# Kernel optimization log

Measured on AMD Instinct MI355X. Metric: run time of the kernel, lower is better.

## Reference

```python
import jax, jax.numpy as jnp
import numpy as np

NEG_SLOPE = 0.2
EPS = 1e-16


def _add_self_loops(edge_index, num_nodes):
    loop = jnp.arange(num_nodes, dtype=edge_index.dtype)
    return jnp.concatenate([edge_index, jnp.stack([loop, loop])], axis=1)


def gat_conv(x, edge_index, W, a_src, a_dst, b, concat):
    """PyG-style GATConv: gather -> attention logits -> segment softmax -> scatter-add."""
    N = x.shape[0]
    H, C = a_src.shape
    xl = (x @ W).reshape(N, H, C)                       # [N,H,C]
    alpha_src = (xl * a_src[None]).sum(-1)              # [N,H]
    alpha_dst = (xl * a_dst[None]).sum(-1)              # [N,H]
    src, dst = edge_index[0], edge_index[1]
    alpha = jax.nn.leaky_relu(alpha_src[src] + alpha_dst[dst], NEG_SLOPE)  # [E,H]
    amax = jax.ops.segment_max(alpha, dst, num_segments=N)
    amax = jnp.where(jnp.isfinite(amax), amax, 0.0)
    ea = jnp.exp(alpha - amax[dst])
    denom = jax.ops.segment_sum(ea, dst, num_segments=N)
    attn = ea / (denom[dst] + EPS)                      # [E,H]
    msg = xl[src] * attn[:, :, None]                    # [E,H,C]
    out = jax.ops.segment_sum(msg, dst, num_segments=N)  # [N,H,C]
    out = out.reshape(N, H * C) if concat else out.mean(axis=1)
    return out + b


def setup_inputs() -> dict:
    key = jax.random.key(0)
    ks = jax.random.split(key, 9)
    N, F, E, H, C, NC = 100000, 128, 1600000, 8, 8, 40
    s = lambda fan: 1.0 / np.sqrt(fan)
    return {
        "x": jax.random.normal(ks[0], (N, F), dtype=jnp.float32),
        "edge_index": jax.random.randint(ks[1], (2, E), 0, N, dtype=jnp.int64),
        "W1": jax.random.normal(ks[2], (F, H * C), dtype=jnp.float32) * s(F),
        "a_src1": jax.random.normal(ks[3], (H, C), dtype=jnp.float32) * s(C),
        "a_dst1": jax.random.normal(ks[4], (H, C), dtype=jnp.float32) * s(C),
        "b1": jnp.zeros((H * C,), dtype=jnp.float32),
        "W2": jax.random.normal(ks[5], (H * C, NC), dtype=jnp.float32) * s(H * C),
        "a_src2": jax.random.normal(ks[6], (1, NC), dtype=jnp.float32) * s(NC),
        "a_dst2": jax.random.normal(ks[7], (1, NC), dtype=jnp.float32) * s(NC),
        "b2": jnp.zeros((NC,), dtype=jnp.float32),
    }


def reference(x, edge_index, W1, a_src1, a_dst1, b1, W2, a_src2, a_dst2, b2):
    N = x.shape[0]
    ei = _add_self_loops(edge_index, N)
    h = gat_conv(x, ei, W1, a_src1, a_dst1, b1, concat=True)   # [N,64]
    h = jax.nn.elu(h)
    out = gat_conv(h, ei, W2, a_src2, a_dst2, b2, concat=True)  # [N,nclass]
    return out
```

## Files before the change

kernel.cpp:

```cpp
#include <hip/hip_runtime.h>
#include <math.h>

#define NEG_SLOPE 0.2f
#define GAT_EPS 1e-16f
#define LOG2E 1.44269504088896340736f

#define CH   2048
#define NBK  512

__device__ __forceinline__ unsigned pack_bf16(float a, float b) {
    unsigned ua = __float_as_uint(a);
    unsigned ub = __float_as_uint(b);
    ua = (ua + 0x8000u) >> 16;
    ub = (ub + 0x8000u) & 0xffff0000u;
    return ua | ub;
}
__device__ __forceinline__ float bf_lo(unsigned pk) {
    return __uint_as_float(pk << 16);
}
__device__ __forceinline__ float bf_hi(unsigned pk) {
    return __uint_as_float(pk & 0xffff0000u);
}


__global__ __launch_bounds__(256) void k_off_a(
    const int* __restrict__ cnt, int* __restrict__ off,
    int* __restrict__ tot, int NCHv)
{
    __shared__ int sm[256];
    int b = blockIdx.x;
    int t = threadIdx.x;
    int carry = 0;
    for (int c0 = 0; c0 < NCHv; c0 += 256) {
        int c = c0 + t;
        int v = (c < NCHv) ? cnt[c * NBK + b] : 0;
        sm[t] = v;
        __syncthreads();
        for (int o = 1; o < 256; o <<= 1) {
            int add = (t >= o) ? sm[t - o] : 0;
            __syncthreads();
            sm[t] += add;
            __syncthreads();
        }
        if (c < NCHv) off[c * NBK + b] = carry + sm[t] - v;
        carry += sm[255];
        __syncthreads();
    }
    if (t == 0) tot[b] = carry;
}

__global__ __launch_bounds__(256) void k_place(
    const int* __restrict__ ei, int E, int N, int shift,
    const int* __restrict__ off, const int* __restrict__ tot,
    unsigned* __restrict__ bslab)
{
    __shared__ int cur[NBK];
    __shared__ int ps[256];
    int c = blockIdx.x;
    int t = threadIdx.x;
    int carry = 0;
    for (int b0 = 0; b0 < NBK; b0 += 256) {
        int v = tot[b0 + t];
        ps[t] = v;
        __syncthreads();
        for (int o = 1; o < 256; o <<= 1) {
            int u = (t >= o) ? ps[t - o] : 0;
            __syncthreads();
            ps[t] += u;
            __syncthreads();
        }
        cur[b0 + t] = carry + ps[t] - v + off[(size_t)c * NBK + b0 + t];
        carry += ps[255];
        __syncthreads();
    }
    __syncthreads();

    int Etot = E + N;
    int base = c * CH;
    int lim = min(base + CH, Etot);
    int mask = (1 << shift) - 1;
    for (int e = base + t; e < lim; e += 256) {
        int s, d;
        if (e < E) { s = ei[e]; d = ei[E + e]; }
        else       { s = e - E; d = s; }
        int b = d >> shift;
        int pos = atomicAdd(&cur[b], 1);
        bslab[pos] = (unsigned)s | ((unsigned)(d & mask) << 17);
    }
}

__global__ __launch_bounds__(256) void k_csr2(
    const int* __restrict__ tot, const unsigned* __restrict__ bslab,
    int shift, int* __restrict__ row_ptr, int* __restrict__ csr_src,
    int N, int Etot)
{
    __shared__ int sdeg[1024];
    __shared__ int scur[1024];
    __shared__ int ps[256];
    __shared__ int bb[NBK + 1];
    int b = blockIdx.x;
    int tid = threadIdx.x;

    int carry = 0;
    for (int b0 = 0; b0 < NBK; b0 += 256) {
        int v = tot[b0 + tid];
        ps[tid] = v;
        __syncthreads();
        for (int o = 1; o < 256; o <<= 1) {
            int u = (tid >= o) ? ps[tid - o] : 0;
            __syncthreads();
            ps[tid] += u;
            __syncthreads();
        }
        bb[b0 + tid] = carry + ps[tid] - v;
        carry += ps[255];
        __syncthreads();
    }
    if (tid == 0) bb[NBK] = carry;
    __syncthreads();

    int beg = bb[b], end = bb[b + 1];
    int nodes = 1 << shift;
    int node0 = b << shift;
    for (int i = tid; i < nodes; i += 256) sdeg[i] = 0;
    __syncthreads();
    for (int i = beg + tid; i < end; i += 256)
        atomicAdd(&sdeg[bslab[i] >> 17], 1);
    __syncthreads();
    int per = (nodes + 255) / 256;
    int mybase = tid * per;
    int sum = 0;
    for (int j = 0; j < per; j++) sum += sdeg[mybase + j];
    ps[tid] = sum;
    __syncthreads();
    int v0 = ps[tid];
    for (int o = 1; o < 256; o <<= 1) {
        int v = (tid >= o) ? ps[tid - o] : 0;
        __syncthreads();
        ps[tid] += v;
        __syncthreads();
    }
    int run = ps[tid] - v0;
    for (int j = 0; j < per; j++) {
        int i = mybase + j;
        int dgi = sdeg[i];
        scur[i] = beg + run;
        int node = node0 + i;
        if (node < N) row_ptr[node] = beg + run;
        run += dgi;
    }
    if (b == 0 && tid == 0) row_ptr[N] = Etot;
    __syncthreads();
    for (int i = beg + tid; i < end; i += 256) {
        unsigned w = bslab[i];
        int pos = atomicAdd(&scur[w >> 17], 1);
        csr_src[pos] = (int)(w & 0x1FFFFu);
    }
}

__device__ __forceinline__ void emit_node1(
    const float* acc, int n, int q, int c0,
    const float* asrc, const float* adst,
    unsigned* __restrict__ xl1b, float* __restrict__ as1,
    float* __restrict__ ad1)
{
    uint4 pk0, pk1;
    pk0.x = pack_bf16(acc[0], acc[1]);  pk0.y = pack_bf16(acc[2], acc[3]);
    pk0.z = pack_bf16(acc[4], acc[5]);  pk0.w = pack_bf16(acc[6], acc[7]);
    pk1.x = pack_bf16(acc[8], acc[9]);  pk1.y = pack_bf16(acc[10], acc[11]);
    pk1.z = pack_bf16(acc[12], acc[13]); pk1.w = pack_bf16(acc[14], acc[15]);
    uint4* xo = (uint4*)(xl1b + (size_t)n * 32 + q * 8);
    xo[0] = pk0;
    xo[1] = pk1;
#pragma unroll
    for (int hh = 0; hh < 2; hh++) {
        float s = 0.0f, t = 0.0f;
#pragma unroll
        for (int c = 0; c < 8; c++) {
            s = fmaf(acc[hh * 8 + c], asrc[c0 + hh * 8 + c], s);
            t = fmaf(acc[hh * 8 + c], adst[c0 + hh * 8 + c], t);
        }
        as1[(size_t)n * 8 + 2 * q + hh] = s * LOG2E;
        ad1[(size_t)n * 8 + 2 * q + hh] = t * LOG2E;
    }
}

__global__ __launch_bounds__(256) void k_gemm1(
    const float* __restrict__ x, const float* __restrict__ W1,
    const float* __restrict__ a_src1, const float* __restrict__ a_dst1,
    unsigned* __restrict__ xl1b, float* __restrict__ as1,
    float* __restrict__ ad1, int N, int F,
    const int* __restrict__ ei, int E, int shift, int NCHv,
    int* __restrict__ cnt)
{
    __shared__ float Ws[128 * 64];
    __shared__ float asrc[64];
    __shared__ float adst[64];
    __shared__ int hist[NBK];

    if (blockIdx.x < NCHv) {
        for (int i = threadIdx.x; i < NBK; i += 256) hist[i] = 0;
        __syncthreads();
        int Etot = E + N;
        int base = blockIdx.x * CH;
        int lim = min(base + CH, Etot);
        for (int e = base + threadIdx.x; e < lim; e += 256) {
            int d = (e < E) ? ei[E + e] : (e - E);
            atomicAdd(&hist[d >> shift], 1);
        }
        __syncthreads();
        for (int i = threadIdx.x; i < NBK; i += 256)
            cnt[(size_t)blockIdx.x * NBK + i] = hist[i];
    }
    if (blockIdx.x * 256 >= N) return;

    for (int i = threadIdx.x; i < F * 64; i += 256) Ws[i] = W1[i];
    if (threadIdx.x < 64) {
        asrc[threadIdx.x] = a_src1[threadIdx.x];
        adst[threadIdx.x] = a_dst1[threadIdx.x];
    }
    __syncthreads();

    int q = threadIdx.x & 3;
    int n0 = blockIdx.x * 256 + (threadIdx.x >> 2) * 4;
    if (n0 >= N) return;
    int c0 = q * 16;
    int n1 = min(n0 + 1, N - 1);
    int n2 = min(n0 + 2, N - 1);
    int n3 = min(n0 + 3, N - 1);

    float acc0[16], acc1[16], acc2[16], acc3[16];
#pragma unroll
    for (int c = 0; c < 16; c++) { acc0[c]=0.f; acc1[c]=0.f; acc2[c]=0.f; acc3[c]=0.f; }

    const float4* xr0 = (const float4*)(x + (size_t)n0 * F);
    const float4* xr1 = (const float4*)(x + (size_t)n1 * F);
    const float4* xr2 = (const float4*)(x + (size_t)n2 * F);
    const float4* xr3 = (const float4*)(x + (size_t)n3 * F);

#define GEMM1_ROW(comp, ridx)                                        \
    { const float* w = &Ws[(k4 * 4 + ridx) * 64 + c0];               \
      _Pragma("unroll")                                              \
      for (int c = 0; c < 16; c++) {                                 \
          float wc = w[c];                                           \
          acc0[c] = fmaf(xv0.comp, wc, acc0[c]);                     \
          acc1[c] = fmaf(xv1.comp, wc, acc1[c]);                     \
          acc2[c] = fmaf(xv2.comp, wc, acc2[c]);                     \
          acc3[c] = fmaf(xv3.comp, wc, acc3[c]); } }

    for (int k4 = 0; k4 < F / 4; k4++) {
        float4 xv0 = xr0[k4];
        float4 xv1 = xr1[k4];
        float4 xv2 = xr2[k4];
        float4 xv3 = xr3[k4];
        GEMM1_ROW(x, 0)
        GEMM1_ROW(y, 1)
        GEMM1_ROW(z, 2)
        GEMM1_ROW(w, 3)
    }
#undef GEMM1_ROW

    emit_node1(acc0, n0, q, c0, asrc, adst, xl1b, as1, ad1);
    if (n0 + 1 < N) emit_node1(acc1, n0 + 1, q, c0, asrc, adst, xl1b, as1, ad1);
    if (n0 + 2 < N) emit_node1(acc2, n0 + 2, q, c0, asrc, adst, xl1b, as1, ad1);
    if (n0 + 3 < N) emit_node1(acc3, n0 + 3, q, c0, asrc, adst, xl1b, as1, ad1);
}

__global__ __launch_bounds__(256) void k_agg1(
    const int* __restrict__ row_ptr, const int* __restrict__ csr_src,
    const float* __restrict__ as1, const float* __restrict__ ad1,
    const unsigned* __restrict__ xl1b, const float* __restrict__ b1,
    float* __restrict__ h1, int N)
{
    int d = blockIdx.x * 8 + ((threadIdx.x >> 6) << 1) + ((threadIdx.x >> 5) & 1);
    if (d >= N) return;
    int lane = threadIdx.x & 31;
    int g = lane >> 3;
    int l = lane & 7;

    int beg = row_ptr[d], end = row_ptr[d + 1];
    float adh = ad1[(size_t)d * 8 + l];

    float ax[8];
#pragma unroll
    for (int j = 0; j < 8; j++) ax[j] = 0.f;
    float den = 0.f;

    int i = beg + g;
    for (; i + 4 < end; i += 8) {
        int s0 = csr_src[i];
        int s1 = csr_src[i + 4];
        size_t q0 = (size_t)s0 * 8 + l;
        size_t q1 = (size_t)s1 * 8 + l;
        float al0 = as1[q0] + adh;
        float al1 = as1[q1] + adh;
        uint4 k0 = *(const uint4*)(xl1b + (q0 << 2));
        uint4 k1 = *(const uint4*)(xl1b + (q1 << 2));
        al0 = fmaxf(al0, NEG_SLOPE * al0);
        al1 = fmaxf(al1, NEG_SLOPE * al1);
        float e0 = __builtin_amdgcn_exp2f(al0);
        float e1 = __builtin_amdgcn_exp2f(al1);
        ax[0] = fmaf(e0, bf_lo(k0.x), ax[0]);
        ax[1] = fmaf(e0, bf_hi(k0.x), ax[1]);
        ax[2] = fmaf(e0, bf_lo(k0.y), ax[2]);
        ax[3] = fmaf(e0, bf_hi(k0.y), ax[3]);
        ax[4] = fmaf(e0, bf_lo(k0.z), ax[4]);
        ax[5] = fmaf(e0, bf_hi(k0.z), ax[5]);
        ax[6] = fmaf(e0, bf_lo(k0.w), ax[6]);
        ax[7] = fmaf(e0, bf_hi(k0.w), ax[7]);
        ax[0] = fmaf(e1, bf_lo(k1.x), ax[0]);
        ax[1] = fmaf(e1, bf_hi(k1.x), ax[1]);
        ax[2] = fmaf(e1, bf_lo(k1.y), ax[2]);
        ax[3] = fmaf(e1, bf_hi(k1.y), ax[3]);
        ax[4] = fmaf(e1, bf_lo(k1.z), ax[4]);
        ax[5] = fmaf(e1, bf_hi(k1.z), ax[5]);
        ax[6] = fmaf(e1, bf_lo(k1.w), ax[6]);
        ax[7] = fmaf(e1, bf_hi(k1.w), ax[7]);
        den += e0 + e1;
    }
    if (i < end) {
        int s0 = csr_src[i];
        size_t q0 = (size_t)s0 * 8 + l;
        float al0 = as1[q0] + adh;
        uint4 k0 = *(const uint4*)(xl1b + (q0 << 2));
        al0 = fmaxf(al0, NEG_SLOPE * al0);
        float e0 = __builtin_amdgcn_exp2f(al0);
        ax[0] = fmaf(e0, bf_lo(k0.x), ax[0]);
        ax[1] = fmaf(e0, bf_hi(k0.x), ax[1]);
        ax[2] = fmaf(e0, bf_lo(k0.y), ax[2]);
        ax[3] = fmaf(e0, bf_hi(k0.y), ax[3]);
        ax[4] = fmaf(e0, bf_lo(k0.z), ax[4]);
        ax[5] = fmaf(e0, bf_hi(k0.z), ax[5]);
        ax[6] = fmaf(e0, bf_lo(k0.w), ax[6]);
        ax[7] = fmaf(e0, bf_hi(k0.w), ax[7]);
        den += e0;
    }

#pragma unroll
    for (int m = 8; m < 32; m <<= 1) {
#pragma unroll
        for (int j = 0; j < 8; j++) ax[j] += __shfl_xor(ax[j], m);
        den += __shfl_xor(den, m);
    }

    if (g == 0) {
        float inv = __builtin_amdgcn_rcpf(den + GAT_EPS);
        const float4* bb = (const float4*)(b1 + l * 8);
        float4 b0 = bb[0], b1v = bb[1];
        float4 o0, o1;
        float v;
        v = fmaf(ax[0], inv, b0.x);  o0.x = v > 0.f ? v : __expf(v) - 1.f;
        v = fmaf(ax[1], inv, b0.y);  o0.y = v > 0.f ? v : __expf(v) - 1.f;
        v = fmaf(ax[2], inv, b0.z);  o0.z = v > 0.f ? v : __expf(v) - 1.f;
        v = fmaf(ax[3], inv, b0.w);  o0.w = v > 0.f ? v : __expf(v) - 1.f;
        v = fmaf(ax[4], inv, b1v.x); o1.x = v > 0.f ? v : __expf(v) - 1.f;
        v = fmaf(ax[5], inv, b1v.y); o1.y = v > 0.f ? v : __expf(v) - 1.f;
        v = fmaf(ax[6], inv, b1v.z); o1.z = v > 0.f ? v : __expf(v) - 1.f;
        v = fmaf(ax[7], inv, b1v.w); o1.w = v > 0.f ? v : __expf(v) - 1.f;
        float4* op = (float4*)(h1 + (size_t)d * 64 + l * 8);
        op[0] = o0;
        op[1] = o1;
    }
}

__global__ __launch_bounds__(256) void k_node2(
    const float* __restrict__ h1, const float* __restrict__ W2,
    const float* __restrict__ a_src2, const float* __restrict__ a_dst2,
    unsigned* __restrict__ xl2b, float* __restrict__ ad2, int N)
{
    __shared__ float Ws[64 * 40];
    __shared__ float a2s[40];
    __shared__ float a2d[40];
    for (int i = threadIdx.x; i < 64 * 40; i += 256) Ws[i] = W2[i];
    if (threadIdx.x < 40) {
        a2s[threadIdx.x] = a_src2[threadIdx.x];
        a2d[threadIdx.x] = a_dst2[threadIdx.x];
    }
    __syncthreads();

    int q = threadIdx.x & 1;
    int n0 = blockIdx.x * 256 + (threadIdx.x >> 1) * 2;
    if (n0 >= N) return;
    int c0 = q * 20;
    int n1 = min(n0 + 1, N - 1);

    float o0[20], o1[20];
#pragma unroll
    for (int j = 0; j < 20; j++) { o0[j] = 0.f; o1[j] = 0.f; }

    const float4* hr0 = (const float4*)(h1 + (size_t)n0 * 64);
    const float4* hr1 = (const float4*)(h1 + (size_t)n1 * 64);

#define NODE2_ROW(comp, ridx)                                        \
    { const float* w = &Ws[(k4 * 4 + ridx) * 40 + c0];               \
      _Pragma("unroll")                                              \
      for (int j = 0; j < 20; j++) {                                 \
          float wj = w[j];                                           \
          o0[j] = fmaf(ha.comp, wj, o0[j]);                          \
          o1[j] = fmaf(hb.comp, wj, o1[j]); } }

    for (int k4 = 0; k4 < 16; k4++) {
        float4 ha = hr0[k4];
        float4 hb = hr1[k4];
        NODE2_ROW(x, 0)
        NODE2_ROW(y, 1)
        NODE2_ROW(z, 2)
        NODE2_ROW(w, 3)
    }
#undef NODE2_ROW

    float s0 = 0.f, t0 = 0.f, s1 = 0.f, t1 = 0.f;
#pragma unroll
    for (int j = 0; j < 20; j++) {
        s0 = fmaf(o0[j], a2s[c0 + j], s0);
        t0 = fmaf(o0[j], a2d[c0 + j], t0);
        s1 = fmaf(o1[j], a2s[c0 + j], s1);
        t1 = fmaf(o1[j], a2d[c0 + j], t1);
    }
    s0 += __shfl_xor(s0, 1);
    t0 += __shfl_xor(t0, 1);
    s1 += __shfl_xor(s1, 1);
    t1 += __shfl_xor(t1, 1);
    if (q == 0) {
        xl2b[(size_t)n0 * 24 + 20] = __float_as_uint(s0 * LOG2E);
        ad2[n0] = t0 * LOG2E;
        if (n0 + 1 < N) {
            xl2b[(size_t)(n0 + 1) * 24 + 20] = __float_as_uint(s1 * LOG2E);
            ad2[n0 + 1] = t1 * LOG2E;
        }
    }

    unsigned* xo0 = xl2b + (size_t)n0 * 24 + q * 10;
#pragma unroll
    for (int p = 0; p < 10; p++) xo0[p] = pack_bf16(o0[2 * p], o0[2 * p + 1]);
    if (n0 + 1 < N) {
        unsigned* xo1 = xl2b + (size_t)(n0 + 1) * 24 + q * 10;
#pragma unroll
        for (int p = 0; p < 10; p++) xo1[p] = pack_bf16(o1[2 * p], o1[2 * p + 1]);
    }
}

__global__ __launch_bounds__(256) void k_agg2(
    const int* __restrict__ row_ptr, const int* __restrict__ csr_src,
    const float* __restrict__ ad2,
    const unsigned* __restrict__ xl2b, const float* __restrict__ b2,
    float* __restrict__ out, int N)
{
    int d = blockIdx.x * 8 + ((threadIdx.x >> 6) << 1) + ((threadIdx.x >> 5) & 1);
    if (d >= N) return;
    int lane = threadIdx.x & 31;
    int g = lane >> 3;
    int l = lane & 7;
    if (l >= 5) return;

    int beg = row_ptr[d], end = row_ptr[d + 1];
    float add = ad2[d];

    float ax[8];
#pragma unroll
    for (int j = 0; j < 8; j++) ax[j] = 0.f;
    float den = 0.f;

    int i = beg + g;
    for (; i + 4 < end; i += 8) {
        int s0 = csr_src[i];
        int s1 = csr_src[i + 4];
        const unsigned* r0 = xl2b + (size_t)s0 * 24;
        const unsigned* r1 = xl2b + (size_t)s1 * 24;
        float al0 = __uint_as_float(r0[20]) + add;
        float al1 = __uint_as_float(r1[20]) + add;
        uint4 k0 = *(const uint4*)(r0 + l * 4);
        uint4 k1 = *(const uint4*)(r1 + l * 4);
        al0 = fmaxf(al0, NEG_SLOPE * al0);
        al1 = fmaxf(al1, NEG_SLOPE * al1);
        float e0 = __builtin_amdgcn_exp2f(al0);
        float e1 = __builtin_amdgcn_exp2f(al1);
        ax[0] = fmaf(e0, bf_lo(k0.x), ax[0]);
        ax[1] = fmaf(e0, bf_hi(k0.x), ax[1]);
        ax[2] = fmaf(e0, bf_lo(k0.y), ax[2]);
        ax[3] = fmaf(e0, bf_hi(k0.y), ax[3]);
        ax[4] = fmaf(e0, bf_lo(k0.z), ax[4]);
        ax[5] = fmaf(e0, bf_hi(k0.z), ax[5]);
        ax[6] = fmaf(e0, bf_lo(k0.w), ax[6]);
        ax[7] = fmaf(e0, bf_hi(k0.w), ax[7]);
        ax[0] = fmaf(e1, bf_lo(k1.x), ax[0]);
        ax[1] = fmaf(e1, bf_hi(k1.x), ax[1]);
        ax[2] = fmaf(e1, bf_lo(k1.y), ax[2]);
        ax[3] = fmaf(e1, bf_hi(k1.y), ax[3]);
        ax[4] = fmaf(e1, bf_lo(k1.z), ax[4]);
        ax[5] = fmaf(e1, bf_hi(k1.z), ax[5]);
        ax[6] = fmaf(e1, bf_lo(k1.w), ax[6]);
        ax[7] = fmaf(e1, bf_hi(k1.w), ax[7]);
        den += e0 + e1;
    }
    if (i < end) {
        int s0 = csr_src[i];
        const unsigned* r0 = xl2b + (size_t)s0 * 24;
        float al0 = __uint_as_float(r0[20]) + add;
        uint4 k0 = *(const uint4*)(r0 + l * 4);
        al0 = fmaxf(al0, NEG_SLOPE * al0);
        float e0 = __builtin_amdgcn_exp2f(al0);
        ax[0] = fmaf(e0, bf_lo(k0.x), ax[0]);
        ax[1] = fmaf(e0, bf_hi(k0.x), ax[1]);
        ax[2] = fmaf(e0, bf_lo(k0.y), ax[2]);
        ax[3] = fmaf(e0, bf_hi(k0.y), ax[3]);
        ax[4] = fmaf(e0, bf_lo(k0.z), ax[4]);
        ax[5] = fmaf(e0, bf_hi(k0.z), ax[5]);
        ax[6] = fmaf(e0, bf_lo(k0.w), ax[6]);
        ax[7] = fmaf(e0, bf_hi(k0.w), ax[7]);
        den += e0;
    }

#pragma unroll
    for (int m = 8; m < 32; m <<= 1) {
#pragma unroll
        for (int j = 0; j < 8; j++) ax[j] += __shfl_xor(ax[j], m);
        den += __shfl_xor(den, m);
    }

    if (g == 0) {
        float inv = __builtin_amdgcn_rcpf(den + GAT_EPS);
        float* op = out + (size_t)d * 40 + l * 8;
        const float* bb = b2 + l * 8;
#pragma unroll
        for (int j = 0; j < 8; j++) op[j] = fmaf(ax[j], inv, bb[j]);
    }
}

extern "C" void kernel_launch(void* const* d_in, const int* in_sizes, int n_in,
                              void* d_out, int out_size, void* d_ws, size_t ws_size,
                              hipStream_t stream) {
    const float* x      = (const float*)d_in[0];
    const int*   ei     = (const int*)d_in[1];
    const float* W1     = (const float*)d_in[2];
    const float* a_src1 = (const float*)d_in[3];
    const float* a_dst1 = (const float*)d_in[4];
    const float* b1     = (const float*)d_in[5];
    const float* W2     = (const float*)d_in[6];
    const float* a_src2 = (const float*)d_in[7];
    const float* a_dst2 = (const float*)d_in[8];
    const float* b2     = (const float*)d_in[9];

    int F = in_sizes[2] / 64;
    int N = in_sizes[0] / F;
    int E = in_sizes[1] / 2;
    int Etot = E + N;
    int NCHv = (Etot + CH - 1) / CH;
    int shift = 8;
    while (((N - 1) >> shift) >= NBK) shift++;

    unsigned* xl1b    = (unsigned*)d_ws;
    float*    h1      = (float*)(xl1b + (size_t)N * 32);
    float*    as1     = h1 + (size_t)N * 64;
    float*    ad1     = as1 + (size_t)N * 8;
    int*      row_ptr = (int*)(ad1 + (size_t)N * 8);
    int*      csr_src = row_ptr + (N + 1);
    unsigned* bslab   = (unsigned*)(csr_src + Etot);
    int*      cnt     = (int*)h1;
    int*      off     = cnt + (size_t)NCHv * NBK;
    int*      tot     = off + (size_t)NCHv * NBK;
    unsigned* xl2b    = xl1b;
    float*    ad2     = ad1;

    int gridG1 = (N + 255) / 256;
    if (gridG1 < NCHv) gridG1 = NCHv;
    k_gemm1<<<gridG1, 256, 0, stream>>>(x, W1, a_src1, a_dst1,
                                        xl1b, as1, ad1, N, F,
                                        ei, E, shift, NCHv, cnt);

    k_off_a<<<NBK, 256, 0, stream>>>(cnt, off, tot, NCHv);
    k_place<<<NCHv, 256, 0, stream>>>(ei, E, N, shift, off, tot, bslab);
    k_csr2 <<<NBK, 256, 0, stream>>>(tot, bslab, shift,
                                     row_ptr, csr_src, N, Etot);

    k_agg1 <<<(N + 7) / 8, 256, 0, stream>>>(row_ptr, csr_src, as1, ad1,
                                             xl1b, b1, h1, N);

    k_node2<<<(N + 255) / 256, 256, 0, stream>>>(h1, W2, a_src2, a_dst2,
                                                 xl2b, ad2, N);
    k_agg2 <<<(N + 7) / 8, 256, 0, stream>>>(row_ptr, csr_src, ad2,
                                             xl2b, b2, (float*)d_out, N);
}
```

Before: 293.0 us.

## Replace bucketed two-level CSR build with global-atomic degree count and scatter

Swaps the two-pass bucket sort (per-chunk histograms, offset scan, slab placement, per-bucket local sort) for a direct CSR build. Per-node degrees are counted with global atomics inside the first GEMM kernel, followed by a three-kernel scan and a scatter that uses one global atomicAdd per edge on a per-node cursor. This drops the intermediate slab and the extra pass over it, at the cost of many contended global atomics and a nondeterministic neighbor order within rows. It also adds a memset and more small kernel launches.

```diff
diff --git a/kernel.cpp b/kernel.cpp
--- a/kernel.cpp
+++ b/kernel.cpp
@@ -4,9 +4,6 @@
 #define NEG_SLOPE 0.2f
 #define GAT_EPS 1e-16f
 #define LOG2E 1.44269504088896340736f
-
-#define CH   2048
-#define NBK  512
 
 __device__ __forceinline__ unsigned pack_bf16(float a, float b) {
     unsigned ua = __float_as_uint(a);
@@ -23,138 +20,69 @@
 }
 
 
-__global__ __launch_bounds__(256) void k_off_a(
-    const int* __restrict__ cnt, int* __restrict__ off,
-    int* __restrict__ tot, int NCHv)
+__global__ __launch_bounds__(256) void k_scan1(
+    const int* __restrict__ deg, int* __restrict__ row_ptr,
+    int* __restrict__ bsum, int N)
 {
     __shared__ int sm[256];
-    int b = blockIdx.x;
     int t = threadIdx.x;
-    int carry = 0;
-    for (int c0 = 0; c0 < NCHv; c0 += 256) {
-        int c = c0 + t;
-        int v = (c < NCHv) ? cnt[c * NBK + b] : 0;
-        sm[t] = v;
+    int d = blockIdx.x * 256 + t;
+    int v = (d < N) ? deg[d] + 1 : 0;
+    sm[t] = v;
+    __syncthreads();
+    for (int o = 1; o < 256; o <<= 1) {
+        int u = (t >= o) ? sm[t - o] : 0;
         __syncthreads();
-        for (int o = 1; o < 256; o <<= 1) {
-            int add = (t >= o) ? sm[t - o] : 0;
-            __syncthreads();
-            sm[t] += add;
-            __syncthreads();
-        }
-        if (c < NCHv) off[c * NBK + b] = carry + sm[t] - v;
-        carry += sm[255];
+        sm[t] += u;
         __syncthreads();
     }
-    if (t == 0) tot[b] = carry;
-}
-
-__global__ __launch_bounds__(256) void k_place(
-    const int* __restrict__ ei, int E, int N, int shift,
-    const int* __restrict__ off, const int* __restrict__ tot,
-    unsigned* __restrict__ bslab)
-{
-    __shared__ int cur[NBK];
-    __shared__ int ps[256];
-    int c = blockIdx.x;
+    if (d < N) row_ptr[d] = sm[t] - v;
+    if (t == 255) bsum[blockIdx.x] = sm[255];
+}
+
+__global__ __launch_bounds__(512) void k_scan2(
+    const int* __restrict__ bsum, int* __restrict__ bases, int NB,
+    int* __restrict__ row_ptr, int N, int Etot)
+{
+    __shared__ int sm[512];
     int t = threadIdx.x;
-    int carry = 0;
-    for (int b0 = 0; b0 < NBK; b0 += 256) {
-        int v = tot[b0 + t];
-        ps[t] = v;
+    int v = (t < NB) ? bsum[t] : 0;
+    sm[t] = v;
+    __syncthreads();
+    for (int o = 1; o < 512; o <<= 1) {
+        int u = (t >= o) ? sm[t - o] : 0;
         __syncthreads();
-        for (int o = 1; o < 256; o <<= 1) {
-            int u = (t >= o) ? ps[t - o] : 0;
-            __syncthreads();
-            ps[t] += u;
-            __syncthreads();
-        }
-        cur[b0 + t] = carry + ps[t] - v + off[(size_t)c * NBK + b0 + t];
-        carry += ps[255];
+        sm[t] += u;
         __syncthreads();
     }
-    __syncthreads();
-
+    if (t < NB) bases[t] = sm[t] - v;
+    if (t == 0) row_ptr[N] = Etot;
+}
+
+__global__ __launch_bounds__(256) void k_fix(
+    const int* __restrict__ bases, int* __restrict__ row_ptr,
+    int* __restrict__ cur, int N)
+{
+    int d = blockIdx.x * 256 + threadIdx.x;
+    if (d < N) {
+        int r = bases[blockIdx.x] + row_ptr[d];
+        row_ptr[d] = r;
+        cur[d] = r;
+    }
+}
+
+__global__ __launch_bounds__(256) void k_scatter(
+    const int* __restrict__ ei, int E, int N,
+    int* __restrict__ cur, int* __restrict__ csr_src)
+{
     int Etot = E + N;
-    int base = c * CH;
-    int lim = min(base + CH, Etot);
-    int mask = (1 << shift) - 1;
-    for (int e = base + t; e < lim; e += 256) {
+    int stride = gridDim.x * 256;
+    for (int e = blockIdx.x * 256 + threadIdx.x; e < Etot; e += stride) {
         int s, d;
         if (e < E) { s = ei[e]; d = ei[E + e]; }
         else       { s = e - E; d = s; }
-        int b = d >> shift;
-        int pos = atomicAdd(&cur[b], 1);
-        bslab[pos] = (unsigned)s | ((unsigned)(d & mask) << 17);
-    }
-}
-
-__global__ __launch_bounds__(256) void k_csr2(
-    const int* __restrict__ tot, const unsigned* __restrict__ bslab,
-    int shift, int* __restrict__ row_ptr, int* __restrict__ csr_src,
-    int N, int Etot)
-{
-    __shared__ int sdeg[1024];
-    __shared__ int scur[1024];
-    __shared__ int ps[256];
-    __shared__ int bb[NBK + 1];
-    int b = blockIdx.x;
-    int tid = threadIdx.x;
-
-    int carry = 0;
-    for (int b0 = 0; b0 < NBK; b0 += 256) {
-        int v = tot[b0 + tid];
-        ps[tid] = v;
-        __syncthreads();
-        for (int o = 1; o < 256; o <<= 1) {
-            int u = (tid >= o) ? ps[tid - o] : 0;
-            __syncthreads();
-            ps[tid] += u;
-            __syncthreads();
-        }
-        bb[b0 + tid] = carry + ps[tid] - v;
-        carry += ps[255];
-        __syncthreads();
-    }
-    if (tid == 0) bb[NBK] = carry;
-    __syncthreads();
-
-    int beg = bb[b], end = bb[b + 1];
-    int nodes = 1 << shift;
-    int node0 = b << shift;
-    for (int i = tid; i < nodes; i += 256) sdeg[i] = 0;
-    __syncthreads();
-    for (int i = beg + tid; i < end; i += 256)
-        atomicAdd(&sdeg[bslab[i] >> 17], 1);
-    __syncthreads();
-    int per = (nodes + 255) / 256;
-    int mybase = tid * per;
-    int sum = 0;
-    for (int j = 0; j < per; j++) sum += sdeg[mybase + j];
-    ps[tid] = sum;
-    __syncthreads();
-    int v0 = ps[tid];
-    for (int o = 1; o < 256; o <<= 1) {
-        int v = (tid >= o) ? ps[tid - o] : 0;
-        __syncthreads();
-        ps[tid] += v;
-        __syncthreads();
-    }
-    int run = ps[tid] - v0;
-    for (int j = 0; j < per; j++) {
-        int i = mybase + j;
-        int dgi = sdeg[i];
-        scur[i] = beg + run;
-        int node = node0 + i;
-        if (node < N) row_ptr[node] = beg + run;
-        run += dgi;
-    }
-    if (b == 0 && tid == 0) row_ptr[N] = Etot;
-    __syncthreads();
-    for (int i = beg + tid; i < end; i += 256) {
-        unsigned w = bslab[i];
-        int pos = atomicAdd(&scur[w >> 17], 1);
-        csr_src[pos] = (int)(w & 0x1FFFFu);
+        int pos = atomicAdd(&cur[d], 1);
+        csr_src[pos] = s;
     }
 }
 
@@ -190,29 +118,19 @@
     const float* __restrict__ a_src1, const float* __restrict__ a_dst1,
     unsigned* __restrict__ xl1b, float* __restrict__ as1,
     float* __restrict__ ad1, int N, int F,
-    const int* __restrict__ ei, int E, int shift, int NCHv,
-    int* __restrict__ cnt)
+    const int* __restrict__ ei, int E, int* __restrict__ deg)
 {
     __shared__ float Ws[128 * 64];
     __shared__ float asrc[64];
     __shared__ float adst[64];
-    __shared__ int hist[NBK];
-
-    if (blockIdx.x < NCHv) {
-        for (int i = threadIdx.x; i < NBK; i += 256) hist[i] = 0;
-        __syncthreads();
-        int Etot = E + N;
-        int base = blockIdx.x * CH;
-        int lim = min(base + CH, Etot);
-        for (int e = base + threadIdx.x; e < lim; e += 256) {
-            int d = (e < E) ? ei[E + e] : (e - E);
-            atomicAdd(&hist[d >> shift], 1);
-        }
-        __syncthreads();
-        for (int i = threadIdx.x; i < NBK; i += 256)
-            cnt[(size_t)blockIdx.x * NBK + i] = hist[i];
-    }
-    if (blockIdx.x * 256 >= N) return;
+
+    {
+        int per = (E + (int)gridDim.x - 1) / (int)gridDim.x;
+        int base = blockIdx.x * per;
+        int lim = min(base + per, E);
+        for (int e = base + threadIdx.x; e < lim; e += 256)
+            atomicAdd(&deg[ei[E + e]], 1);
+    }
 
     for (int i = threadIdx.x; i < F * 64; i += 256) Ws[i] = W1[i];
     if (threadIdx.x < 64) {
@@ -545,9 +463,7 @@
     int N = in_sizes[0] / F;
     int E = in_sizes[1] / 2;
     int Etot = E + N;
-    int NCHv = (Etot + CH - 1) / CH;
-    int shift = 8;
-    while (((N - 1) >> shift) >= NBK) shift++;
+    int NB = (N + 255) / 256;
 
     unsigned* xl1b    = (unsigned*)d_ws;
     float*    h1      = (float*)(xl1b + (size_t)N * 32);
@@ -555,29 +471,31 @@
     float*    ad1     = as1 + (size_t)N * 8;
     int*      row_ptr = (int*)(ad1 + (size_t)N * 8);
     int*      csr_src = row_ptr + (N + 1);
-    unsigned* bslab   = (unsigned*)(csr_src + Etot);
-    int*      cnt     = (int*)h1;
-    int*      off     = cnt + (size_t)NCHv * NBK;
-    int*      tot     = off + (size_t)NCHv * NBK;
+    int*      deg     = csr_src + Etot;
+    int*      cur     = deg + N;
+    int*      bsum    = cur + N;
+    int*      bases   = bsum + NB;
     unsigned* xl2b    = xl1b;
     float*    ad2     = ad1;
 
-    int gridG1 = (N + 255) / 256;
-    if (gridG1 < NCHv) gridG1 = NCHv;
-    k_gemm1<<<gridG1, 256, 0, stream>>>(x, W1, a_src1, a_dst1,
-                                        xl1b, as1, ad1, N, F,
-                                        ei, E, shift, NCHv, cnt);
-
-    k_off_a<<<NBK, 256, 0, stream>>>(cnt, off, tot, NCHv);
-    k_place<<<NCHv, 256, 0, stream>>>(ei, E, N, shift, off, tot, bslab);
-    k_csr2 <<<NBK, 256, 0, stream>>>(tot, bslab, shift,
-                                     row_ptr, csr_src, N, Etot);
+    hipMemsetAsync(deg, 0, (size_t)N * sizeof(int), stream);
+
+    k_gemm1<<<NB, 256, 0, stream>>>(x, W1, a_src1, a_dst1,
+                                    xl1b, as1, ad1, N, F, ei, E, deg);
+
+    k_scan1<<<NB, 256, 0, stream>>>(deg, row_ptr, bsum, N);
+    k_scan2<<<1, 512, 0, stream>>>(bsum, bases, NB, row_ptr, N, Etot);
+    k_fix  <<<NB, 256, 0, stream>>>(bases, row_ptr, cur, N);
+    {
+        int gs = (Etot + 255) / 256;
+        if (gs > 2048) gs = 2048;
+        k_scatter<<<gs, 256, 0, stream>>>(ei, E, N, cur, csr_src);
+    }
 
     k_agg1 <<<(N + 7) / 8, 256, 0, stream>>>(row_ptr, csr_src, as1, ad1,
                                              xl1b, b1, h1, N);
 
-    k_node2<<<(N + 255) / 256, 256, 0, stream>>>(h1, W2, a_src2, a_dst2,
-                                                 xl2b, ad2, N);
+    k_node2<<<NB, 256, 0, stream>>>(h1, W2, a_src2, a_dst2, xl2b, ad2, N);
     k_agg2 <<<(N + 7) / 8, 256, 0, stream>>>(row_ptr, csr_src, ad2,
                                              xl2b, b2, (float*)d_out, N);
 }
```

Result: slower. 450.7 us (+53.8%).

## Fuse layer-2 linear projection into layer-1 aggregation epilogue

Applied to the files above, without the earlier changes.

Merges the k_node2 GEMM into the end of k_agg1. Each 32-lane destination group applies bias and ELU, multiplies by W2 held in shared memory, and reduces partial sums with shuffles to produce bf16 xl2 rows and the attention logits. This removes the fp32 h1 round-trip through global memory and one kernel launch. The cost is a W2 load into LDS in every small 8-node block, extra shuffle reductions, and xl2b/ad2 moving to separate workspace regions so they no longer alias xl1b and ad1 while those are still being read.

```diff
diff --git a/kernel.cpp b/kernel.cpp
--- a/kernel.cpp
+++ b/kernel.cpp
@@ -270,8 +270,22 @@
     const int* __restrict__ row_ptr, const int* __restrict__ csr_src,
     const float* __restrict__ as1, const float* __restrict__ ad1,
     const unsigned* __restrict__ xl1b, const float* __restrict__ b1,
-    float* __restrict__ h1, int N)
-{
+    const float* __restrict__ W2, const float* __restrict__ a_src2,
+    const float* __restrict__ a_dst2,
+    unsigned* __restrict__ xl2b, float* __restrict__ ad2, int N)
+{
+    __shared__ float W2s[64 * 40];
+    __shared__ float b1s[64];
+    __shared__ float a2ss[40];
+    __shared__ float a2ds[40];
+    for (int i = threadIdx.x; i < 64 * 40; i += 256) W2s[i] = W2[i];
+    if (threadIdx.x < 64) b1s[threadIdx.x] = b1[threadIdx.x];
+    if (threadIdx.x < 40) {
+        a2ss[threadIdx.x] = a_src2[threadIdx.x];
+        a2ds[threadIdx.x] = a_dst2[threadIdx.x];
+    }
+    __syncthreads();
+
     int d = blockIdx.x * 8 + ((threadIdx.x >> 6) << 1) + ((threadIdx.x >> 5) & 1);
     if (d >= N) return;
     int lane = threadIdx.x & 31;
@@ -343,100 +357,49 @@
         den += __shfl_xor(den, m);
     }
 
-    if (g == 0) {
-        float inv = __builtin_amdgcn_rcpf(den + GAT_EPS);
-        const float4* bb = (const float4*)(b1 + l * 8);
-        float4 b0 = bb[0], b1v = bb[1];
-        float4 o0, o1;
-        float v;
-        v = fmaf(ax[0], inv, b0.x);  o0.x = v > 0.f ? v : __expf(v) - 1.f;
-        v = fmaf(ax[1], inv, b0.y);  o0.y = v > 0.f ? v : __expf(v) - 1.f;
-        v = fmaf(ax[2], inv, b0.z);  o0.z = v > 0.f ? v : __expf(v) - 1.f;
-        v = fmaf(ax[3], inv, b0.w);  o0.w = v > 0.f ? v : __expf(v) - 1.f;
-        v = fmaf(ax[4], inv, b1v.x); o1.x = v > 0.f ? v : __expf(v) - 1.f;
-        v = fmaf(ax[5], inv, b1v.y); o1.y = v > 0.f ? v : __expf(v) - 1.f;
-        v = fmaf(ax[6], inv, b1v.z); o1.z = v > 0.f ? v : __expf(v) - 1.f;
-        v = fmaf(ax[7], inv, b1v.w); o1.w = v > 0.f ? v : __expf(v) - 1.f;
-        float4* op = (float4*)(h1 + (size_t)d * 64 + l * 8);
-        op[0] = o0;
-        op[1] = o1;
-    }
-}
-
-__global__ __launch_bounds__(256) void k_node2(
-    const float* __restrict__ h1, const float* __restrict__ W2,
-    const float* __restrict__ a_src2, const float* __restrict__ a_dst2,
-    unsigned* __restrict__ xl2b, float* __restrict__ ad2, int N)
-{
-    __shared__ float Ws[64 * 40];
-    __shared__ float a2s[40];
-    __shared__ float a2d[40];
-    for (int i = threadIdx.x; i < 64 * 40; i += 256) Ws[i] = W2[i];
-    if (threadIdx.x < 40) {
-        a2s[threadIdx.x] = a_src2[threadIdx.x];
-        a2d[threadIdx.x] = a_dst2[threadIdx.x];
-    }
-    __syncthreads();
-
-    int q = threadIdx.x & 1;
-    int n0 = blockIdx.x * 256 + (threadIdx.x >> 1) * 2;
-    if (n0 >= N) return;
-    int c0 = q * 20;
-    int n1 = min(n0 + 1, N - 1);
-
-    float o0[20], o1[20];
-#pragma unroll
-    for (int j = 0; j < 20; j++) { o0[j] = 0.f; o1[j] = 0.f; }
-
-    const float4* hr0 = (const float4*)(h1 + (size_t)n0 * 64);
-    const float4* hr1 = (const float4*)(h1 + (size_t)n1 * 64);
-
-#define NODE2_ROW(comp, ridx)                                        \
-    { const float* w = &Ws[(k4 * 4 + ridx) * 40 + c0];               \
-      _Pragma("unroll")                                              \
-      for (int j = 0; j < 20; j++) {                                 \
-          float wj = w[j];                                           \
-          o0[j] = fmaf(ha.comp, wj, o0[j]);                          \
-          o1[j] = fmaf(hb.comp, wj, o1[j]); } }
-
-    for (int k4 = 0; k4 < 16; k4++) {
-        float4 ha = hr0[k4];
-        float4 hb = hr1[k4];
-        NODE2_ROW(x, 0)
-        NODE2_ROW(y, 1)
-        NODE2_ROW(z, 2)
-        NODE2_ROW(w, 3)
-    }
-#undef NODE2_ROW
-
-    float s0 = 0.f, t0 = 0.f, s1 = 0.f, t1 = 0.f;
-#pragma unroll
-    for (int j = 0; j < 20; j++) {
-        s0 = fmaf(o0[j], a2s[c0 + j], s0);
-        t0 = fmaf(o0[j], a2d[c0 + j], t0);
-        s1 = fmaf(o1[j], a2s[c0 + j], s1);
-        t1 = fmaf(o1[j], a2d[c0 + j], t1);
-    }
-    s0 += __shfl_xor(s0, 1);
-    t0 += __shfl_xor(t0, 1);
-    s1 += __shfl_xor(s1, 1);
-    t1 += __shfl_xor(t1, 1);
-    if (q == 0) {
-        xl2b[(size_t)n0 * 24 + 20] = __float_as_uint(s0 * LOG2E);
-        ad2[n0] = t0 * LOG2E;
-        if (n0 + 1 < N) {
-            xl2b[(size_t)(n0 + 1) * 24 + 20] = __float_as_uint(s1 * LOG2E);
-            ad2[n0 + 1] = t1 * LOG2E;
+    float inv = __builtin_amdgcn_rcpf(den + GAT_EPS);
+    float h[8];
+#pragma unroll
+    for (int j = 0; j < 8; j++) {
+        float v = fmaf(ax[j], inv, b1s[l * 8 + j]);
+        h[j] = v > 0.f ? v : __expf(v) - 1.f;
+    }
+
+    float pt[10];
+#pragma unroll
+    for (int jj = 0; jj < 10; jj++) pt[jj] = 0.f;
+#pragma unroll
+    for (int c = 0; c < 8; c++) {
+        float hc = h[c];
+        const float* wr = &W2s[(l * 8 + c) * 40 + g * 10];
+#pragma unroll
+        for (int jj = 0; jj < 10; jj++) pt[jj] = fmaf(hc, wr[jj], pt[jj]);
+    }
+#pragma unroll
+    for (int m = 1; m < 8; m <<= 1) {
+#pragma unroll
+        for (int jj = 0; jj < 10; jj++) pt[jj] += __shfl_xor(pt[jj], m);
+    }
+    float s2 = 0.f, t2 = 0.f;
+#pragma unroll
+    for (int jj = 0; jj < 10; jj++) {
+        s2 = fmaf(pt[jj], a2ss[g * 10 + jj], s2);
+        t2 = fmaf(pt[jj], a2ds[g * 10 + jj], t2);
+    }
+    s2 += __shfl_xor(s2, 8);  s2 += __shfl_xor(s2, 16);
+    t2 += __shfl_xor(t2, 8);  t2 += __shfl_xor(t2, 16);
+
+    if (l == 0) {
+        unsigned* xo = xl2b + (size_t)d * 24 + g * 5;
+        xo[0] = pack_bf16(pt[0], pt[1]);
+        xo[1] = pack_bf16(pt[2], pt[3]);
+        xo[2] = pack_bf16(pt[4], pt[5]);
+        xo[3] = pack_bf16(pt[6], pt[7]);
+        xo[4] = pack_bf16(pt[8], pt[9]);
+        if (g == 0) {
+            xl2b[(size_t)d * 24 + 20] = __float_as_uint(s2 * LOG2E);
+            ad2[d] = t2 * LOG2E;
         }
-    }
-
-    unsigned* xo0 = xl2b + (size_t)n0 * 24 + q * 10;
-#pragma unroll
-    for (int p = 0; p < 10; p++) xo0[p] = pack_bf16(o0[2 * p], o0[2 * p + 1]);
-    if (n0 + 1 < N) {
-        unsigned* xo1 = xl2b + (size_t)(n0 + 1) * 24 + q * 10;
-#pragma unroll
-        for (int p = 0; p < 10; p++) xo1[p] = pack_bf16(o1[2 * p], o1[2 * p + 1]);
     }
 }
 
@@ -550,17 +513,16 @@
     while (((N - 1) >> shift) >= NBK) shift++;
 
     unsigned* xl1b    = (unsigned*)d_ws;
-    float*    h1      = (float*)(xl1b + (size_t)N * 32);
-    float*    as1     = h1 + (size_t)N * 64;
+    float*    as1     = (float*)(xl1b + (size_t)N * 32);
     float*    ad1     = as1 + (size_t)N * 8;
     int*      row_ptr = (int*)(ad1 + (size_t)N * 8);
     int*      csr_src = row_ptr + (N + 1);
     unsigned* bslab   = (unsigned*)(csr_src + Etot);
-    int*      cnt     = (int*)h1;
+    int*      cnt     = (int*)(bslab + Etot);
     int*      off     = cnt + (size_t)NCHv * NBK;
     int*      tot     = off + (size_t)NCHv * NBK;
-    unsigned* xl2b    = xl1b;
-    float*    ad2     = ad1;
+    unsigned* xl2b    = (unsigned*)(tot + NBK);
+    float*    ad2     = (float*)(xl2b + (size_t)N * 24);
 
     int gridG1 = (N + 255) / 256;
     if (gridG1 < NCHv) gridG1 = NCHv;
@@ -574,10 +536,9 @@
                                      row_ptr, csr_src, N, Etot);
 
     k_agg1 <<<(N + 7) / 8, 256, 0, stream>>>(row_ptr, csr_src, as1, ad1,
-                                             xl1b, b1, h1, N);
-
-    k_node2<<<(N + 255) / 256, 256, 0, stream>>>(h1, W2, a_src2, a_dst2,
-                                                 xl2b, ad2, N);
+                                             xl1b, b1, W2, a_src2, a_dst2,
+                                             xl2b, ad2, N);
+
     k_agg2 <<<(N + 7) / 8, 256, 0, stream>>>(row_ptr, csr_src, ad2,
                                              xl2b, b2, (float*)d_out, N);
 }
```

Result: slower. 384.1 us (+31.1%).

## Replace per-chunk offset scan with global bucket atomics and single-block scan

Applied to the files above, without the earlier changes.

Drops the per-chunk count matrix and its column scans. Per-chunk histograms now go into padded global bucket totals via atomics, one small block scans them into bucket bases, and k_place claims each chunk's range in a bucket with one global atomic per nonempty bucket after staging its edges in shared memory. This removes the k_off_a pass, the redundant prefix scans repeated in every k_place and k_csr2 block, and the NCHv x NBK count traffic. k_csr2 is also launched only over the buckets actually used. In exchange it adds a memset and makes edge order within a bucket nondeterministic, which can change the floating-point summation order.

```diff
diff --git a/kernel.cpp b/kernel.cpp
--- a/kernel.cpp
+++ b/kernel.cpp
@@ -7,6 +7,7 @@
 
 #define CH   2048
 #define NBK  512
+#define TOTS 16
 
 __device__ __forceinline__ unsigned pack_bf16(float a, float b) {
     unsigned ua = __float_as_uint(a);
@@ -23,103 +24,77 @@
 }
 
 
-__global__ __launch_bounds__(256) void k_off_a(
-    const int* __restrict__ cnt, int* __restrict__ off,
-    int* __restrict__ tot, int NCHv)
-{
-    __shared__ int sm[256];
-    int b = blockIdx.x;
+__global__ __launch_bounds__(NBK) void k_scan(
+    const int* __restrict__ totp, int* __restrict__ bbase,
+    int* __restrict__ gcur)
+{
+    __shared__ int sm[NBK];
     int t = threadIdx.x;
-    int carry = 0;
-    for (int c0 = 0; c0 < NCHv; c0 += 256) {
-        int c = c0 + t;
-        int v = (c < NCHv) ? cnt[c * NBK + b] : 0;
-        sm[t] = v;
+    int v = totp[t * TOTS];
+    sm[t] = v;
+    __syncthreads();
+    for (int o = 1; o < NBK; o <<= 1) {
+        int u = (t >= o) ? sm[t - o] : 0;
         __syncthreads();
-        for (int o = 1; o < 256; o <<= 1) {
-            int add = (t >= o) ? sm[t - o] : 0;
-            __syncthreads();
-            sm[t] += add;
-            __syncthreads();
-        }
-        if (c < NCHv) off[c * NBK + b] = carry + sm[t] - v;
-        carry += sm[255];
+        sm[t] += u;
         __syncthreads();
     }
-    if (t == 0) tot[b] = carry;
+    int ex = sm[t] - v;
+    bbase[t] = ex;
+    gcur[t * TOTS] = ex;
+    if (t == NBK - 1) bbase[NBK] = sm[t];
 }
 
 __global__ __launch_bounds__(256) void k_place(
     const int* __restrict__ ei, int E, int N, int shift,
-    const int* __restrict__ off, const int* __restrict__ tot,
-    unsigned* __restrict__ bslab)
-{
-    __shared__ int cur[NBK];
-    __shared__ int ps[256];
-    int c = blockIdx.x;
-    int t = threadIdx.x;
-    int carry = 0;
-    for (int b0 = 0; b0 < NBK; b0 += 256) {
-        int v = tot[b0 + t];
-        ps[t] = v;
-        __syncthreads();
-        for (int o = 1; o < 256; o <<= 1) {
-            int u = (t >= o) ? ps[t - o] : 0;
-            __syncthreads();
-            ps[t] += u;
-            __syncthreads();
-        }
-        cur[b0 + t] = carry + ps[t] - v + off[(size_t)c * NBK + b0 + t];
-        carry += ps[255];
-        __syncthreads();
-    }
-    __syncthreads();
-
+    int* __restrict__ gcur, unsigned* __restrict__ bslab)
+{
+    __shared__ unsigned sew[CH];
+    __shared__ unsigned short seb[CH];
+    __shared__ int hist[NBK];
+    __shared__ int curb[NBK];
+    int c = blockIdx.x, t = threadIdx.x;
+    for (int i = t; i < NBK; i += 256) hist[i] = 0;
+    __syncthreads();
     int Etot = E + N;
     int base = c * CH;
     int lim = min(base + CH, Etot);
+    int n = lim - base;
     int mask = (1 << shift) - 1;
-    for (int e = base + t; e < lim; e += 256) {
+    for (int i = t; i < n; i += 256) {
+        int e = base + i;
         int s, d;
         if (e < E) { s = ei[e]; d = ei[E + e]; }
         else       { s = e - E; d = s; }
         int b = d >> shift;
-        int pos = atomicAdd(&cur[b], 1);
-        bslab[pos] = (unsigned)s | ((unsigned)(d & mask) << 17);
+        sew[i] = (unsigned)s | ((unsigned)(d & mask) << 17);
+        seb[i] = (unsigned short)b;
+        atomicAdd(&hist[b], 1);
+    }
+    __syncthreads();
+    for (int b = t; b < NBK; b += 256) {
+        int h = hist[b];
+        curb[b] = h ? atomicAdd(&gcur[b * TOTS], h) : 0;
+    }
+    __syncthreads();
+    for (int i = t; i < n; i += 256) {
+        int b = seb[i];
+        int pos = atomicAdd(&curb[b], 1);
+        bslab[pos] = sew[i];
     }
 }
 
 __global__ __launch_bounds__(256) void k_csr2(
-    const int* __restrict__ tot, const unsigned* __restrict__ bslab,
+    const int* __restrict__ bbase, const unsigned* __restrict__ bslab,
     int shift, int* __restrict__ row_ptr, int* __restrict__ csr_src,
     int N, int Etot)
 {
     __shared__ int sdeg[1024];
     __shared__ int scur[1024];
     __shared__ int ps[256];
-    __shared__ int bb[NBK + 1];
     int b = blockIdx.x;
     int tid = threadIdx.x;
-
-    int carry = 0;
-    for (int b0 = 0; b0 < NBK; b0 += 256) {
-        int v = tot[b0 + tid];
-        ps[tid] = v;
-        __syncthreads();
-        for (int o = 1; o < 256; o <<= 1) {
-            int u = (tid >= o) ? ps[tid - o] : 0;
-            __syncthreads();
-            ps[tid] += u;
-            __syncthreads();
-        }
-        bb[b0 + tid] = carry + ps[tid] - v;
-        carry += ps[255];
-        __syncthreads();
-    }
-    if (tid == 0) bb[NBK] = carry;
-    __syncthreads();
-
-    int beg = bb[b], end = bb[b + 1];
+    int beg = bbase[b], end = bbase[b + 1];
     int nodes = 1 << shift;
     int node0 = b << shift;
     for (int i = tid; i < nodes; i += 256) sdeg[i] = 0;
@@ -191,7 +166,7 @@
     unsigned* __restrict__ xl1b, float* __restrict__ as1,
     float* __restrict__ ad1, int N, int F,
     const int* __restrict__ ei, int E, int shift, int NCHv,
-    int* __restrict__ cnt)
+    int* __restrict__ totp)
 {
     __shared__ float Ws[128 * 64];
     __shared__ float asrc[64];
@@ -209,8 +184,10 @@
             atomicAdd(&hist[d >> shift], 1);
         }
         __syncthreads();
-        for (int i = threadIdx.x; i < NBK; i += 256)
-            cnt[(size_t)blockIdx.x * NBK + i] = hist[i];
+        for (int i = threadIdx.x; i < NBK; i += 256) {
+            int h = hist[i];
+            if (h) atomicAdd(&totp[i * TOTS], h);
+        }
     }
     if (blockIdx.x * 256 >= N) return;
 
@@ -548,6 +525,7 @@
     int NCHv = (Etot + CH - 1) / CH;
     int shift = 8;
     while (((N - 1) >> shift) >= NBK) shift++;
+    int NBused = ((N + (1 << shift) - 1) >> shift);
 
     unsigned* xl1b    = (unsigned*)d_ws;
     float*    h1      = (float*)(xl1b + (size_t)N * 32);
@@ -556,22 +534,24 @@
     int*      row_ptr = (int*)(ad1 + (size_t)N * 8);
     int*      csr_src = row_ptr + (N + 1);
     unsigned* bslab   = (unsigned*)(csr_src + Etot);
-    int*      cnt     = (int*)h1;
-    int*      off     = cnt + (size_t)NCHv * NBK;
-    int*      tot     = off + (size_t)NCHv * NBK;
+    int*      totp    = (int*)(bslab + Etot);
+    int*      gcur    = totp + (size_t)NBK * TOTS;
+    int*      bbase   = gcur + (size_t)NBK * TOTS;
     unsigned* xl2b    = xl1b;
     float*    ad2     = ad1;
+
+    hipMemsetAsync(totp, 0, (size_t)NBK * TOTS * sizeof(int), stream);
 
     int gridG1 = (N + 255) / 256;
     if (gridG1 < NCHv) gridG1 = NCHv;
     k_gemm1<<<gridG1, 256, 0, stream>>>(x, W1, a_src1, a_dst1,
                                         xl1b, as1, ad1, N, F,
-                                        ei, E, shift, NCHv, cnt);
-
-    k_off_a<<<NBK, 256, 0, stream>>>(cnt, off, tot, NCHv);
-    k_place<<<NCHv, 256, 0, stream>>>(ei, E, N, shift, off, tot, bslab);
-    k_csr2 <<<NBK, 256, 0, stream>>>(tot, bslab, shift,
-                                     row_ptr, csr_src, N, Etot);
+                                        ei, E, shift, NCHv, totp);
+
+    k_scan <<<1, NBK, 0, stream>>>(totp, bbase, gcur);
+    k_place<<<NCHv, 256, 0, stream>>>(ei, E, N, shift, gcur, bslab);
+    k_csr2 <<<NBused, 256, 0, stream>>>(bbase, bslab, shift,
+                                        row_ptr, csr_src, N, Etot);
 
     k_agg1 <<<(N + 7) / 8, 256, 0, stream>>>(row_ptr, csr_src, as1, ad1,
                                              xl1b, b1, h1, N);
```

Result: slower. 316.7 us (+8.1%).
